# Kernel tuning notes

Measured on AMD Instinct MI355X. Metric: run time of the kernel, lower is better.

The kernel has to match this reference:

```python
import jax, jax.numpy as jnp
import numpy as np
from jax import lax

# ---- module hyperparams (match init_kwargs and mamba_ssm Mamba2 defaults) ----
D_MODEL = 768
D_STATE = 64
D_CONV = 4
EXPAND = 2
HEADDIM = 64  # Mamba2 default
D_INNER = EXPAND * D_MODEL          # 1536
NHEADS = D_INNER // HEADDIM         # 24
NGROUPS = 1
CONV_DIM = D_INNER + 2 * NGROUPS * D_STATE          # 1664
D_IN_PROJ = 2 * D_INNER + 2 * NGROUPS * D_STATE + NHEADS  # 3224
BSZ, SEQ = 2, 512
EPS = 1e-5


def setup_inputs() -> dict:
    key = jax.random.key(0)
    ks = jax.random.split(key, 12)
    def n(k, shape, s):
        return jax.random.normal(k, shape, jnp.float32) * s
    x = n(ks[0], (BSZ, SEQ, D_MODEL), 1.0)
    in_proj_w = n(ks[1], (D_IN_PROJ, D_MODEL), D_MODEL ** -0.5)
    conv_w = n(ks[2], (CONV_DIM, D_CONV), D_CONV ** -0.5)
    conv_b = jnp.zeros((CONV_DIM,), jnp.float32)
    # dt_bias = softplus^{-1}(dt) with dt log-uniform in [1e-3, 1e-1] (Mamba2 init)
    dt = jnp.exp(jax.random.uniform(ks[3], (NHEADS,), jnp.float32,
                                    minval=np.log(1e-3), maxval=np.log(1e-1)))
    dt_bias = dt + jnp.log(-jnp.expm1(-dt))
    A_log = jnp.log(jax.random.uniform(ks[4], (NHEADS,), jnp.float32, minval=1.0, maxval=16.0))
    D_param = jnp.ones((NHEADS,), jnp.float32)
    norm_w = jnp.ones((D_INNER,), jnp.float32)
    out_proj_w = n(ks[5], (D_MODEL, D_INNER), D_INNER ** -0.5)
    ln1_w = jnp.ones((D_MODEL,), jnp.float32); ln1_b = jnp.zeros((D_MODEL,), jnp.float32)
    ln2_w = jnp.ones((D_MODEL,), jnp.float32); ln2_b = jnp.zeros((D_MODEL,), jnp.float32)
    ff_w1 = n(ks[6], (4 * D_MODEL, D_MODEL), D_MODEL ** -0.5)
    ff_b1 = jnp.zeros((4 * D_MODEL,), jnp.float32)
    ff_w2 = n(ks[7], (D_MODEL, 4 * D_MODEL), (4 * D_MODEL) ** -0.5)
    ff_b2 = jnp.zeros((D_MODEL,), jnp.float32)
    return dict(x=x, in_proj_w=in_proj_w, conv_w=conv_w, conv_b=conv_b,
                dt_bias=dt_bias, A_log=A_log, D_param=D_param, norm_w=norm_w,
                out_proj_w=out_proj_w, ln1_w=ln1_w, ln1_b=ln1_b,
                ln2_w=ln2_w, ln2_b=ln2_b, ff_w1=ff_w1, ff_b1=ff_b1,
                ff_w2=ff_w2, ff_b2=ff_b2)


def layernorm(x, w, b):
    mu = jnp.mean(x, -1, keepdims=True)
    xc = x - mu
    var = jnp.mean(xc * xc, -1, keepdims=True)
    return xc * lax.rsqrt(var + EPS) * w + b


def mamba2(xn, in_proj_w, conv_w, conv_b, dt_bias, A_log, D_param, norm_w, out_proj_w):
    b, l, _ = xn.shape
    zxbcdt = xn @ in_proj_w.T  # [b, l, D_IN_PROJ]
    z = zxbcdt[..., :D_INNER]
    xBC = zxbcdt[..., D_INNER:D_INNER + CONV_DIM]
    dt = zxbcdt[..., D_INNER + CONV_DIM:]
    # causal depthwise conv over time on xBC
    xc = lax.conv_general_dilated(xBC.transpose(0, 2, 1), conv_w[:, None, :], (1,),
                                  [(D_CONV - 1, 0)], dimension_numbers=('NCH', 'OIH', 'NCH'),
                                  feature_group_count=CONV_DIM)
    xBC = jax.nn.silu((xc + conv_b[None, :, None]).transpose(0, 2, 1))
    xs = xBC[..., :D_INNER].reshape(b, l, NHEADS, HEADDIM)
    Bm = xBC[..., D_INNER:D_INNER + D_STATE]   # [b, l, n]  (ngroups=1)
    Cm = xBC[..., D_INNER + D_STATE:]          # [b, l, n]
    dt = jax.nn.softplus(dt + dt_bias)         # [b, l, h]
    dA = jnp.exp(dt * (-jnp.exp(A_log)))       # [b, l, h]
    dBx = jnp.einsum('blh,bln,blhp->blhpn', dt, Bm, xs)
    def step(h, inp):
        dA_t, dBx_t = inp                      # [b,h], [b,h,p,n]
        h = dA_t[:, :, None, None] * h + dBx_t
        return h, h
    _, hs = lax.scan(step, jnp.zeros((b, NHEADS, HEADDIM, D_STATE), xn.dtype),
                     (dA.transpose(1, 0, 2), dBx.transpose(1, 0, 2, 3, 4)))
    y = jnp.einsum('lbhpn,bln->blhp', hs, Cm) + D_param[None, None, :, None] * xs
    y = y.reshape(b, l, D_INNER) * jax.nn.silu(z)   # gated RMSNorm (norm_before_gate=False)
    y = y * lax.rsqrt(jnp.mean(y * y, -1, keepdims=True) + EPS) * norm_w
    return y @ out_proj_w.T


def reference(x, in_proj_w, conv_w, conv_b, dt_bias, A_log, D_param, norm_w,
              out_proj_w, ln1_w, ln1_b, ln2_w, ln2_b, ff_w1, ff_b1, ff_w2, ff_b2):
    residual = x
    xn = layernorm(x, ln1_w, ln1_b)
    mp = (in_proj_w, conv_w, conv_b, dt_bias, A_log, D_param, norm_w, out_proj_w)
    out_f = mamba2(xn, *mp)
    out_b = jnp.flip(mamba2(jnp.flip(xn, 1), *mp), 1)
    m = layernorm(out_f + out_b, ln2_w, ln2_b)
    ff = jax.nn.gelu(m @ ff_w1.T + ff_b1, approximate=False) @ ff_w2.T + ff_b2
    return ff + residual
```

## Files before the change

kernel.cpp:

```cpp
#include <hip/hip_runtime.h>
#include <hip/hip_bf16.h>
#include <math.h>

#define SEQ     512
#define BSZ     2
#define ROWS    (BSZ*SEQ)
#define DMODEL  768
#define DINNER  1536
#define DSTATE  64
#define NHEADS  24
#define HEADDIM 64
#define CONVDIM 1664
#define DINPROJ 3224
#define DFF     3072
#define EPSF    1e-5f

typedef __attribute__((ext_vector_type(8))) short s16x8;
typedef __attribute__((ext_vector_type(4))) float f32x4;

__device__ __forceinline__ float b2f(const __hip_bfloat16 v){ return __bfloat162float(v); }
__device__ __forceinline__ __hip_bfloat16 f2b(float v){ return __float2bfloat16(v); }
__device__ __forceinline__ ushort f2bu(float v){
  union { __hip_bfloat16 b; ushort u; } c; c.b = __float2bfloat16(v); return c.u;
}
__device__ __forceinline__ float u2f(ushort u){ return __uint_as_float(((uint)u) << 16); }

__device__ __forceinline__ void gload16(const void* g, void* l){
  __builtin_amdgcn_global_load_lds((__attribute__((address_space(1))) const void*)g,
                                   (__attribute__((address_space(3))) void*)l, 16, 0, 0);
}

__device__ __forceinline__ float block_sum256(float v, float* sh){
  #pragma unroll
  for (int off = 32; off > 0; off >>= 1) v += __shfl_down(v, off, 64);
  int w = threadIdx.x >> 6;
  if ((threadIdx.x & 63) == 0) sh[w] = v;
  __syncthreads();
  float t = sh[0] + sh[1] + sh[2] + sh[3];
  __syncthreads();
  return t;
}

__global__ __launch_bounds__(256) void zerof_kernel(float* out, int n){
  int i = blockIdx.x*256 + threadIdx.x;
  if (i < n) out[i] = 0.f;
}

__global__ __launch_bounds__(256) void prep_kernel(const float* __restrict__ w0,
    const float* __restrict__ w1, const float* __restrict__ w2,
    const float* __restrict__ w3, ushort* __restrict__ o,
    int n0, int n1, int n2, int n3, int wblocks,
    const float* __restrict__ xin, const float* __restrict__ lnw,
    const float* __restrict__ lnb, __hip_bfloat16* __restrict__ xnout)
{
  __shared__ float sh[4];
  if ((int)blockIdx.x < wblocks){
    int i = (blockIdx.x*256 + threadIdx.x) << 2;
    int total = n0 + n1 + n2 + n3;
    if (i < total){
      const float* s; int off;
      if      (i < n0)       { s = w0; off = i; }
      else if (i < n0+n1)    { s = w1; off = i - n0; }
      else if (i < n0+n1+n2) { s = w2; off = i - n0 - n1; }
      else                   { s = w3; off = i - n0 - n1 - n2; }
      float4 f = *(const float4*)(s + off);
      *(ushort4*)(o + i) = make_ushort4(f2bu(f.x), f2bu(f.y), f2bu(f.z), f2bu(f.w));
    }
    return;
  }
  const int row = blockIdx.x - wblocks;
  const float* xr = xin + (size_t)row * DMODEL;
  float v[3]; float s = 0.f;
  #pragma unroll
  for (int i = 0; i < 3; i++){ int c = threadIdx.x + i*256; v[i] = xr[c]; s += v[i]; }
  s = block_sum256(s, sh);
  float mu = s * (1.f/DMODEL);
  float s2 = 0.f;
  #pragma unroll
  for (int i = 0; i < 3; i++){ float d = v[i]-mu; s2 += d*d; }
  s2 = block_sum256(s2, sh);
  float rs = rsqrtf(s2*(1.f/DMODEL) + EPSF);
  #pragma unroll
  for (int i = 0; i < 3; i++){
    int c = threadIdx.x + i*256;
    xnout[(size_t)row*DMODEL + c] = f2b((v[i]-mu)*rs*lnw[c] + lnb[c]);
  }
}

__global__ __launch_bounds__(256) void ln_kernel(const float* __restrict__ in,
    const float* __restrict__ w, const float* __restrict__ b,
    __hip_bfloat16* __restrict__ out)
{
  __shared__ float sh[4];
  const int row = blockIdx.x;
  const float* xr = in + (size_t)row * DMODEL;
  float v[3]; float s = 0.f;
  #pragma unroll
  for (int i = 0; i < 3; i++){ int c = threadIdx.x + i*256; v[i] = xr[c]; s += v[i]; }
  s = block_sum256(s, sh);
  float mu = s * (1.f/DMODEL);
  float s2 = 0.f;
  #pragma unroll
  for (int i = 0; i < 3; i++){ float d = v[i]-mu; s2 += d*d; }
  s2 = block_sum256(s2, sh);
  float rs = rsqrtf(s2*(1.f/DMODEL) + EPSF);
  #pragma unroll
  for (int i = 0; i < 3; i++){
    int c = threadIdx.x + i*256;
    out[(size_t)row*DMODEL + c] = f2b((v[i]-mu)*rs*w[c] + b[c]);
  }
}

__device__ __forceinline__ s16x8 ld_frag(const ushort* p){
  union { ushort4 h[2]; s16x8 v; } u;
  u.h[0] = *(const ushort4*)(p);
  u.h[1] = *(const ushort4*)(p + 4);
  return u.v;
}

template<typename CTy, int KS, int EPI>
__global__ __launch_bounds__(256) void gemm_bb64(const __hip_bfloat16* __restrict__ A_,
    const __hip_bfloat16* __restrict__ B_, CTy* __restrict__ C,
    const float* __restrict__ bias, int M, int N, int K)
{
  __shared__ __align__(16) ushort As[3][64][64];
  __shared__ __align__(16) ushort Bs[3][64][64];
  const int tid  = threadIdx.x;
  const int lane = tid & 63, wave = tid >> 6;
  const int wr = wave >> 1, wc = wave & 1;
  const int n0 = blockIdx.x * 64, m0 = blockIdx.y * 64;
  const int Kc   = K / KS;
  const int kbeg = blockIdx.z * Kc;
  const int NT   = Kc >> 6;
  const int srw  = lane >> 3;
  const int scol = (((lane & 7) ^ srw) << 3);
  const int l15  = lane & 15;
  const int r7   = l15 & 7;
  const int c0   = lane >> 4;

  const ushort* Au = (const ushort*)A_;
  const ushort* Bu = (const ushort*)B_;

  f32x4 acc[2][2] = {};

  auto stage = [&](int bf, int k0){
    #pragma unroll
    for (int q = 0; q < 2; q++){
      int row = q*32 + wave*8 + srw;
      gload16(Au + (size_t)(m0 + row)*K + kbeg + k0 + scol, &As[bf][q*32 + wave*8][0]);
      int nr = n0 + row; if (nr > N-1) nr = N-1;
      gload16(Bu + (size_t)nr*K + kbeg + k0 + scol, &Bs[bf][q*32 + wave*8][0]);
    }
  };

  stage(0, 0);
  stage(1, 64);
  asm volatile("s_waitcnt vmcnt(4)" ::: "memory");
  __builtin_amdgcn_s_barrier();

  for (int t = 0; t < NT; ++t){
    const int nxt = t + 2;
    if (nxt < NT) stage(nxt % 3, nxt << 6);
    const int cur = t % 3;
    #pragma unroll
    for (int tt = 0; tt < 2; tt++){
      const int fc = (((tt*4 + c0) ^ r7) << 3);
      s16x8 a0 = ld_frag(&As[cur][wr*32      + l15][fc]);
      s16x8 a1 = ld_frag(&As[cur][wr*32 + 16 + l15][fc]);
      s16x8 b0 = ld_frag(&Bs[cur][wc*32      + l15][fc]);
      s16x8 b1 = ld_frag(&Bs[cur][wc*32 + 16 + l15][fc]);
      acc[0][0] = __builtin_amdgcn_mfma_f32_16x16x32_bf16(a0, b0, acc[0][0], 0, 0, 0);
      acc[0][1] = __builtin_amdgcn_mfma_f32_16x16x32_bf16(a0, b1, acc[0][1], 0, 0, 0);
      acc[1][0] = __builtin_amdgcn_mfma_f32_16x16x32_bf16(a1, b0, acc[1][0], 0, 0, 0);
      acc[1][1] = __builtin_amdgcn_mfma_f32_16x16x32_bf16(a1, b1, acc[1][1], 0, 0, 0);
    }
    if (t == NT-1) break;
    if (nxt < NT) { asm volatile("s_waitcnt vmcnt(4)" ::: "memory"); }
    else          { asm volatile("s_waitcnt vmcnt(0)" ::: "memory"); }
    __builtin_amdgcn_s_barrier();
  }

  CTy* Cz = C + (size_t)blockIdx.z * M * N;
  const int crow = (lane >> 4) * 4;
  #pragma unroll
  for (int i = 0; i < 2; i++){
    #pragma unroll
    for (int j = 0; j < 2; j++){
      int col = n0 + wc*32 + j*16 + l15;
      if (col < N){
        #pragma unroll
        for (int q = 0; q < 4; q++){
          int rowg = m0 + wr*32 + i*16 + crow + q;
          if constexpr (EPI == 1){
            float v = acc[i][j][q] + bias[col];
            Cz[(size_t)rowg*N + col] = (CTy)f2b(0.5f * v * (1.f + erff(v * 0.70710678118654752f)));
          } else if constexpr (sizeof(CTy) == 4){
            Cz[(size_t)rowg*N + col] = acc[i][j][q];
          } else {
            Cz[(size_t)rowg*N + col] = (CTy)f2b(acc[i][j][q]);
          }
        }
      }
    }
  }
}

template<typename CTy>
__global__ __launch_bounds__(256) void gemm_mfma(const __hip_bfloat16* __restrict__ A,
    const float* __restrict__ B, CTy* __restrict__ C, int M, int N, int K)
{
  __shared__ __align__(16) ushort As[64][72];
  __shared__ __align__(16) ushort Bs[64][72];
  const int tid  = threadIdx.x;
  const int lane = tid & 63, wave = tid >> 6;
  const int wr = wave >> 1, wc = wave & 1;
  const int n0 = blockIdx.x * 64, m0 = blockIdx.y * 64;
  const int sr = tid >> 2;
  const int sc = (tid & 3) * 16;
  const int l15 = lane & 15, lk = (lane >> 4) * 8;

  f32x4 acc[2][2] = {};

  const ushort* Au = (const ushort*)A;
  int nr = n0 + sr; if (nr > N-1) nr = N-1;

  for (int k0 = 0; k0 < K; k0 += 64){
    const ushort* ag = Au + (size_t)(m0 + sr)*K + (k0 + sc);
    ushort4 a0 = *(const ushort4*)(ag);
    ushort4 a1 = *(const ushort4*)(ag + 4);
    ushort4 a2 = *(const ushort4*)(ag + 8);
    ushort4 a3 = *(const ushort4*)(ag + 12);
    const float* bg = B + (size_t)nr*K + (k0 + sc);
    float4 f0 = *(const float4*)(bg);
    float4 f1 = *(const float4*)(bg + 4);
    float4 f2 = *(const float4*)(bg + 8);
    float4 f3 = *(const float4*)(bg + 12);
    ushort4 b0 = make_ushort4(f2bu(f0.x), f2bu(f0.y), f2bu(f0.z), f2bu(f0.w));
    ushort4 b1 = make_ushort4(f2bu(f1.x), f2bu(f1.y), f2bu(f1.z), f2bu(f1.w));
    ushort4 b2 = make_ushort4(f2bu(f2.x), f2bu(f2.y), f2bu(f2.z), f2bu(f2.w));
    ushort4 b3 = make_ushort4(f2bu(f3.x), f2bu(f3.y), f2bu(f3.z), f2bu(f3.w));

    __syncthreads();
    *(ushort4*)&As[sr][sc +  0] = a0;
    *(ushort4*)&As[sr][sc +  4] = a1;
    *(ushort4*)&As[sr][sc +  8] = a2;
    *(ushort4*)&As[sr][sc + 12] = a3;
    *(ushort4*)&Bs[sr][sc +  0] = b0;
    *(ushort4*)&Bs[sr][sc +  4] = b1;
    *(ushort4*)&Bs[sr][sc +  8] = b2;
    *(ushort4*)&Bs[sr][sc + 12] = b3;
    __syncthreads();

    #pragma unroll
    for (int kk = 0; kk < 64; kk += 32){
      s16x8 af0 = ld_frag(&As[wr*32      + l15][kk + lk]);
      s16x8 af1 = ld_frag(&As[wr*32 + 16 + l15][kk + lk]);
      s16x8 bf0 = ld_frag(&Bs[wc*32      + l15][kk + lk]);
      s16x8 bf1 = ld_frag(&Bs[wc*32 + 16 + l15][kk + lk]);
      acc[0][0] = __builtin_amdgcn_mfma_f32_16x16x32_bf16(af0, bf0, acc[0][0], 0, 0, 0);
      acc[0][1] = __builtin_amdgcn_mfma_f32_16x16x32_bf16(af0, bf1, acc[0][1], 0, 0, 0);
      acc[1][0] = __builtin_amdgcn_mfma_f32_16x16x32_bf16(af1, bf0, acc[1][0], 0, 0, 0);
      acc[1][1] = __builtin_amdgcn_mfma_f32_16x16x32_bf16(af1, bf1, acc[1][1], 0, 0, 0);
    }
  }

  const int crow = (lane >> 4) * 4;
  #pragma unroll
  for (int i = 0; i < 2; i++){
    #pragma unroll
    for (int j = 0; j < 2; j++){
      int col = n0 + wc*32 + j*16 + l15;
      if (col < N){
        #pragma unroll
        for (int q = 0; q < 4; q++){
          int rowg = m0 + wr*32 + i*16 + crow + q;
          if constexpr (sizeof(CTy) == 4) C[(size_t)rowg*N + col] = acc[i][j][q];
          else                            C[(size_t)rowg*N + col] = (CTy)f2b(acc[i][j][q]);
        }
      }
    }
  }
}

__global__ __launch_bounds__(256) void convdt_kernel(const __hip_bfloat16* __restrict__ zx,
    const float* __restrict__ cw, const float* __restrict__ cb,
    const float* __restrict__ dt_bias, const float* __restrict__ A_log,
    __hip_bfloat16* __restrict__ xconv, float* __restrict__ dtb, float* __restrict__ dab)
{
  const int tt = blockIdx.x, b = blockIdx.y, dir = blockIdx.z;
  const int c8 = threadIdx.x * 8;
  if (c8 < CONVDIM){
    size_t rowoff[4]; bool ok[4];
    #pragma unroll
    for (int k = 0; k < 4; k++){
      int s = tt - 3 + k;
      ok[k] = (s >= 0);
      int ss = ok[k] ? s : 0;
      int phys = dir ? (SEQ-1-ss) : ss;
      rowoff[k] = ((size_t)(b*SEQ + phys))*DINPROJ + DINNER + c8;
    }
    float acc[8];
    {
      float4 cb0 = *(const float4*)(cb + c8);
      float4 cb1 = *(const float4*)(cb + c8 + 4);
      acc[0]=cb0.x; acc[1]=cb0.y; acc[2]=cb0.z; acc[3]=cb0.w;
      acc[4]=cb1.x; acc[5]=cb1.y; acc[6]=cb1.z; acc[7]=cb1.w;
    }
    float wv[8][4];
    #pragma unroll
    for (int j = 0; j < 8; j++){
      float4 w4 = *(const float4*)(cw + (size_t)(c8 + j)*4);
      wv[j][0]=w4.x; wv[j][1]=w4.y; wv[j][2]=w4.z; wv[j][3]=w4.w;
    }
    const ushort* zu = (const ushort*)zx;
    #pragma unroll
    for (int k = 0; k < 4; k++){
      if (ok[k]){
        ushort4 v0 = *(const ushort4*)(zu + rowoff[k]);
        ushort4 v1 = *(const ushort4*)(zu + rowoff[k] + 4);
        acc[0] = fmaf(wv[0][k], u2f(v0.x), acc[0]);
        acc[1] = fmaf(wv[1][k], u2f(v0.y), acc[1]);
        acc[2] = fmaf(wv[2][k], u2f(v0.z), acc[2]);
        acc[3] = fmaf(wv[3][k], u2f(v0.w), acc[3]);
        acc[4] = fmaf(wv[4][k], u2f(v1.x), acc[4]);
        acc[5] = fmaf(wv[5][k], u2f(v1.y), acc[5]);
        acc[6] = fmaf(wv[6][k], u2f(v1.z), acc[6]);
        acc[7] = fmaf(wv[7][k], u2f(v1.w), acc[7]);
      }
    }
    ushort* outr = (ushort*)xconv + ((size_t)((dir*BSZ + b)*SEQ + tt))*CONVDIM + c8;
    ushort o[8];
    #pragma unroll
    for (int j = 0; j < 8; j++){
      float s = acc[j] / (1.f + expf(-acc[j]));
      o[j] = f2bu(s);
    }
    *(ushort4*)(outr)     = make_ushort4(o[0],o[1],o[2],o[3]);
    *(ushort4*)(outr + 4) = make_ushort4(o[4],o[5],o[6],o[7]);
  }
  if (dir == 0 && threadIdx.x < NHEADS){
    int h = threadIdx.x;
    size_t r = (size_t)b*SEQ + tt;
    float raw = b2f(zx[r*DINPROJ + (DINNER + CONVDIM) + h]) + dt_bias[h];
    float sp  = fmaxf(raw, 0.f) + log1pf(expf(-fabsf(raw)));
    dtb[r*NHEADS + h] = sp;
    dab[r*NHEADS + h] = expf(-sp * expf(A_log[h]));
  }
}

#define CT 16

__global__ __launch_bounds__(256) void scan_pass1(const __hip_bfloat16* __restrict__ xconv,
    const float* __restrict__ dtb, const float* __restrict__ dab,
    float* __restrict__ stateBuf, int CL)
{
  const int c = blockIdx.x, h = blockIdx.y, z = blockIdx.z;
  const int b = z & 1, dir = z >> 1;
  const int tid = threadIdx.x, lane = tid & 63, wave = tid >> 6, nb = wave * 16;
  __shared__ __align__(16) float Bc[CT][64], Xc[CT][64];
  __shared__ float dAc[CT], dtc[CT];
  float hreg[16];
  #pragma unroll
  for (int j = 0; j < 16; j++) hreg[j] = 0.f;
  const size_t dirbase = (size_t)z * SEQ;
  const int cstart = c * CL;

  const int ttl = tid >> 4, c4 = (tid & 15) << 2;

  for (int c0 = cstart; c0 < cstart + CL; c0 += CT){
    {
      const ushort* rowp = (const ushort*)xconv + (dirbase + c0 + ttl)*(size_t)CONVDIM;
      ushort4 bv = *(const ushort4*)(rowp + DINNER + c4);
      ushort4 xv = *(const ushort4*)(rowp + h*HEADDIM + c4);
      Bc[ttl][c4+0] = u2f(bv.x); Bc[ttl][c4+1] = u2f(bv.y);
      Bc[ttl][c4+2] = u2f(bv.z); Bc[ttl][c4+3] = u2f(bv.w);
      Xc[ttl][c4+0] = u2f(xv.x); Xc[ttl][c4+1] = u2f(xv.y);
      Xc[ttl][c4+2] = u2f(xv.z); Xc[ttl][c4+3] = u2f(xv.w);
    }
    if (tid < CT){
      int phys = dir ? (SEQ-1 - (c0 + tid)) : (c0 + tid);
      size_t r = (size_t)b*SEQ + phys;
      dAc[tid] = dab[r*NHEADS + h];
      dtc[tid] = dtb[r*NHEADS + h];
    }
    __syncthreads();

    #pragma unroll 4
    for (int tt = 0; tt < CT; tt++){
      float dA = dAc[tt];
      float dtx = dtc[tt] * Xc[tt][lane];
      const float4* Bq = (const float4*)&Bc[tt][nb];
      float4 B0 = Bq[0], B1 = Bq[1], B2 = Bq[2], B3 = Bq[3];
      hreg[ 0]=fmaf(dA,hreg[ 0],dtx*B0.x); hreg[ 1]=fmaf(dA,hreg[ 1],dtx*B0.y);
      hreg[ 2]=fmaf(dA,hreg[ 2],dtx*B0.z); hreg[ 3]=fmaf(dA,hreg[ 3],dtx*B0.w);
      hreg[ 4]=fmaf(dA,hreg[ 4],dtx*B1.x); hreg[ 5]=fmaf(dA,hreg[ 5],dtx*B1.y);
      hreg[ 6]=fmaf(dA,hreg[ 6],dtx*B1.z); hreg[ 7]=fmaf(dA,hreg[ 7],dtx*B1.w);
      hreg[ 8]=fmaf(dA,hreg[ 8],dtx*B2.x); hreg[ 9]=fmaf(dA,hreg[ 9],dtx*B2.y);
      hreg[10]=fmaf(dA,hreg[10],dtx*B2.z); hreg[11]=fmaf(dA,hreg[11],dtx*B2.w);
      hreg[12]=fmaf(dA,hreg[12],dtx*B3.x); hreg[13]=fmaf(dA,hreg[13],dtx*B3.y);
      hreg[14]=fmaf(dA,hreg[14],dtx*B3.z); hreg[15]=fmaf(dA,hreg[15],dtx*B3.w);
    }
    __syncthreads();
  }

  float* sp = stateBuf + (((size_t)c*4 + z)*NHEADS + h)*4096 + (size_t)lane*64 + nb;
  *(float4*)(sp +  0) = make_float4(hreg[ 0],hreg[ 1],hreg[ 2],hreg[ 3]);
  *(float4*)(sp +  4) = make_float4(hreg[ 4],hreg[ 5],hreg[ 6],hreg[ 7]);
  *(float4*)(sp +  8) = make_float4(hreg[ 8],hreg[ 9],hreg[10],hreg[11]);
  *(float4*)(sp + 12) = make_float4(hreg[12],hreg[13],hreg[14],hreg[15]);
}

__global__ __launch_bounds__(256) void scan_pass2(const __hip_bfloat16* __restrict__ xconv,
    const __hip_bfloat16* __restrict__ zx, const float* __restrict__ dtb,
    const float* __restrict__ dab, const float* __restrict__ Dp,
    const float* __restrict__ stateBuf, __hip_bfloat16* __restrict__ yg, int CL)
{
  const int c = blockIdx.x, h = blockIdx.y, z = blockIdx.z;
  const int b = z & 1, dir = z >> 1;
  const int tid = threadIdx.x, lane = tid & 63, wave = tid >> 6, nb = wave * 16;
  __shared__ __align__(16) float Bc[CT][64], Cc[CT][64], Xc[CT][64];
  __shared__ __align__(16) float Yp[4][CT][64];
  __shared__ float dAc[CT], dtc[CT];
  __shared__ float sP[8];
  float hreg[16];
  #pragma unroll
  for (int j = 0; j < 16; j++) hreg[j] = 0.f;
  if (c > 0){
    if (tid < c){
      float p = 1.f;
      for (int i = 0; i < CL; i++){
        int t = tid*CL + i;
        int phys = dir ? (SEQ-1 - t) : t;
        p *= dab[((size_t)b*SEQ + phys)*NHEADS + h];
      }
      sP[tid] = p;
    }
    __syncthreads();
    float suffix = 1.f;
    for (int i = c-1; i >= 0; --i){
      const float* sp = stateBuf + (((size_t)i*4 + z)*NHEADS + h)*4096 + (size_t)lane*64 + nb;
      float4 s0 = *(const float4*)(sp+0), s1 = *(const float4*)(sp+4);
      float4 s2 = *(const float4*)(sp+8), s3 = *(const float4*)(sp+12);
      hreg[ 0]=fmaf(suffix,s0.x,hreg[ 0]); hreg[ 1]=fmaf(suffix,s0.y,hreg[ 1]);
      hreg[ 2]=fmaf(suffix,s0.z,hreg[ 2]); hreg[ 3]=fmaf(suffix,s0.w,hreg[ 3]);
      hreg[ 4]=fmaf(suffix,s1.x,hreg[ 4]); hreg[ 5]=fmaf(suffix,s1.y,hreg[ 5]);
      hreg[ 6]=fmaf(suffix,s1.z,hreg[ 6]); hreg[ 7]=fmaf(suffix,s1.w,hreg[ 7]);
      hreg[ 8]=fmaf(suffix,s2.x,hreg[ 8]); hreg[ 9]=fmaf(suffix,s2.y,hreg[ 9]);
      hreg[10]=fmaf(suffix,s2.z,hreg[10]); hreg[11]=fmaf(suffix,s2.w,hreg[11]);
      hreg[12]=fmaf(suffix,s3.x,hreg[12]); hreg[13]=fmaf(suffix,s3.y,hreg[13]);
      hreg[14]=fmaf(suffix,s3.z,hreg[14]); hreg[15]=fmaf(suffix,s3.w,hreg[15]);
      suffix *= sP[i];
    }
    __syncthreads();
  }
  const float Dh = Dp[h];
  const size_t dirbase = (size_t)z * SEQ;
  const int cstart = c * CL;
  const int ttl = tid >> 4, c4 = (tid & 15) << 2;

  for (int c0 = cstart; c0 < cstart + CL; c0 += CT){
    {
      const ushort* rowp = (const ushort*)xconv + (dirbase + c0 + ttl)*(size_t)CONVDIM;
      ushort4 bv = *(const ushort4*)(rowp + DINNER + c4);
      ushort4 cv = *(const ushort4*)(rowp + DINNER + DSTATE + c4);
      ushort4 xv = *(const ushort4*)(rowp + h*HEADDIM + c4);
      Bc[ttl][c4+0] = u2f(bv.x); Bc[ttl][c4+1] = u2f(bv.y);
      Bc[ttl][c4+2] = u2f(bv.z); Bc[ttl][c4+3] = u2f(bv.w);
      Cc[ttl][c4+0] = u2f(cv.x); Cc[ttl][c4+1] = u2f(cv.y);
      Cc[ttl][c4+2] = u2f(cv.z); Cc[ttl][c4+3] = u2f(cv.w);
      Xc[ttl][c4+0] = u2f(xv.x); Xc[ttl][c4+1] = u2f(xv.y);
      Xc[ttl][c4+2] = u2f(xv.z); Xc[ttl][c4+3] = u2f(xv.w);
    }
    if (tid < CT){
      int phys = dir ? (SEQ-1 - (c0 + tid)) : (c0 + tid);
      size_t r = (size_t)b*SEQ + phys;
      dAc[tid] = dab[r*NHEADS + h];
      dtc[tid] = dtb[r*NHEADS + h];
    }
    __syncthreads();

    #pragma unroll 4
    for (int tt = 0; tt < CT; tt++){
      float dA = dAc[tt];
      float dtx = dtc[tt] * Xc[tt][lane];
      const float4* Bq = (const float4*)&Bc[tt][nb];
      const float4* Cq = (const float4*)&Cc[tt][nb];
      float4 B0 = Bq[0], B1 = Bq[1], B2 = Bq[2], B3 = Bq[3];
      float4 C0 = Cq[0], C1 = Cq[1], C2 = Cq[2], C3 = Cq[3];
      float y0 = 0.f, y1 = 0.f, y2 = 0.f, y3 = 0.f;
      hreg[ 0]=fmaf(dA,hreg[ 0],dtx*B0.x); y0=fmaf(hreg[ 0],C0.x,y0);
      hreg[ 1]=fmaf(dA,hreg[ 1],dtx*B0.y); y1=fmaf(hreg[ 1],C0.y,y1);
      hreg[ 2]=fmaf(dA,hreg[ 2],dtx*B0.z); y2=fmaf(hreg[ 2],C0.z,y2);
      hreg[ 3]=fmaf(dA,hreg[ 3],dtx*B0.w); y3=fmaf(hreg[ 3],C0.w,y3);
      hreg[ 4]=fmaf(dA,hreg[ 4],dtx*B1.x); y0=fmaf(hreg[ 4],C1.x,y0);
      hreg[ 5]=fmaf(dA,hreg[ 5],dtx*B1.y); y1=fmaf(hreg[ 5],C1.y,y1);
      hreg[ 6]=fmaf(dA,hreg[ 6],dtx*B1.z); y2=fmaf(hreg[ 6],C1.z,y2);
      hreg[ 7]=fmaf(dA,hreg[ 7],dtx*B1.w); y3=fmaf(hreg[ 7],C1.w,y3);
      hreg[ 8]=fmaf(dA,hreg[ 8],dtx*B2.x); y0=fmaf(hreg[ 8],C2.x,y0);
      hreg[ 9]=fmaf(dA,hreg[ 9],dtx*B2.y); y1=fmaf(hreg[ 9],C2.y,y1);
      hreg[10]=fmaf(dA,hreg[10],dtx*B2.z); y2=fmaf(hreg[10],C2.z,y2);
      hreg[11]=fmaf(dA,hreg[11],dtx*B2.w); y3=fmaf(hreg[11],C2.w,y3);
      hreg[12]=fmaf(dA,hreg[12],dtx*B3.x); y0=fmaf(hreg[12],C3.x,y0);
      hreg[13]=fmaf(dA,hreg[13],dtx*B3.y); y1=fmaf(hreg[13],C3.y,y1);
      hreg[14]=fmaf(dA,hreg[14],dtx*B3.z); y2=fmaf(hreg[14],C3.z,y2);
      hreg[15]=fmaf(dA,hreg[15],dtx*B3.w); y3=fmaf(hreg[15],C3.w,y3);
      Yp[wave][tt][lane] = (y0+y1) + (y2+y3);
    }
    __syncthreads();

    {
      int tl = tid >> 4, p4 = (tid & 15) << 2;
      float4 ya = *(const float4*)&Yp[0][tl][p4];
      float4 yb4 = *(const float4*)&Yp[1][tl][p4];
      float4 yc = *(const float4*)&Yp[2][tl][p4];
      float4 yd = *(const float4*)&Yp[3][tl][p4];
      float4 xv = *(const float4*)&Xc[tl][p4];
      int phys = dir ? (SEQ-1 - (c0 + tl)) : (c0 + tl);
      size_t r = (size_t)b*SEQ + phys;
      const ushort* zp = (const ushort*)zx + r*DINPROJ + h*HEADDIM + p4;
      ushort4 zv = *(const ushort4*)zp;
      float zf[4] = { u2f(zv.x), u2f(zv.y), u2f(zv.z), u2f(zv.w) };
      float yv[4] = { ya.x+yb4.x+yc.x+yd.x + Dh*xv.x,
                      ya.y+yb4.y+yc.y+yd.y + Dh*xv.y,
                      ya.z+yb4.z+yc.z+yd.z + Dh*xv.z,
                      ya.w+yb4.w+yc.w+yd.w + Dh*xv.w };
      ushort o[4];
      #pragma unroll
      for (int j = 0; j < 4; j++){
        float sil = zf[j] / (1.f + expf(-zf[j]));
        o[j] = f2bu(yv[j] * sil);
      }
      ushort* op = (ushort*)yg + ((size_t)dir*ROWS + r)*DINNER + h*HEADDIM + p4;
      *(ushort4*)op = make_ushort4(o[0],o[1],o[2],o[3]);
    }
    __syncthreads();
  }
}

__global__ __launch_bounds__(256) void rmscomb_kernel(const __hip_bfloat16* __restrict__ yg,
    const float* __restrict__ nw, __hip_bfloat16* __restrict__ u)
{
  __shared__ float sh[4];
  const int row = blockIdx.x;
  const __hip_bfloat16* yf = yg + (size_t)row*DINNER;
  const __hip_bfloat16* yb = yg + (size_t)(ROWS + row)*DINNER;
  float vf[6], vb[6]; float sf = 0.f, sb = 0.f;
  #pragma unroll
  for (int i = 0; i < 6; i++){
    int c = threadIdx.x + i*256;
    vf[i] = b2f(yf[c]); sf += vf[i]*vf[i];
    vb[i] = b2f(yb[c]); sb += vb[i]*vb[i];
  }
  sf = block_sum256(sf, sh);
  sb = block_sum256(sb, sh);
  float rf = rsqrtf(sf*(1.f/DINNER) + EPSF);
  float rb = rsqrtf(sb*(1.f/DINNER) + EPSF);
  #pragma unroll
  for (int i = 0; i < 6; i++){
    int c = threadIdx.x + i*256;
    u[(size_t)row*DINNER + c] = f2b((vf[i]*rf + vb[i]*rb) * nw[c]);
  }
}

template<int NP>
__global__ __launch_bounds__(256) void ln2_kernel(const float* __restrict__ in,
    size_t pstride, const float* __restrict__ w, const float* __restrict__ b,
    __hip_bfloat16* __restrict__ out)
{
  __shared__ float sh[4];
  const int row = blockIdx.x;
  float v[3]; float s = 0.f;
  #pragma unroll
  for (int i = 0; i < 3; i++){
    int c = threadIdx.x + i*256;
    size_t idx = (size_t)row*DMODEL + c;
    float t = 0.f;
    #pragma unroll
    for (int p = 0; p < NP; p++) t += in[p*pstride + idx];
    v[i] = t; s += t;
  }
  s = block_sum256(s, sh);
  float mu = s * (1.f/DMODEL);
  float s2 = 0.f;
  #pragma unroll
  for (int i = 0; i < 3; i++){ float d = v[i]-mu; s2 += d*d; }
  s2 = block_sum256(s2, sh);
  float rs = rsqrtf(s2*(1.f/DMODEL) + EPSF);
  #pragma unroll
  for (int i = 0; i < 3; i++){
    int c = threadIdx.x + i*256;
    out[(size_t)row*DMODEL + c] = f2b((v[i]-mu)*rs*w[c] + b[c]);
  }
}

__global__ __launch_bounds__(256) void gelu_kernel(const __hip_bfloat16* __restrict__ g,
    const float* __restrict__ b1, __hip_bfloat16* __restrict__ out)
{
  size_t idx = (size_t)blockIdx.x*256 + threadIdx.x;
  int c = (int)(idx % DFF);
  float v = b2f(g[idx]) + b1[c];
  out[idx] = f2b(0.5f * v * (1.f + erff(v * 0.70710678118654752f)));
}

template<int NP>
__global__ __launch_bounds__(256) void final_kernel(const float* __restrict__ f,
    size_t pstride, const float* __restrict__ bias, const float* __restrict__ x,
    float* __restrict__ out)
{
  size_t i4 = ((size_t)blockIdx.x*256 + threadIdx.x) << 2;
  int c = (int)(i4 % DMODEL);
  float4 bv = *(const float4*)(bias + c);
  float4 xv = *(const float4*)(x + i4);
  float4 s = make_float4(bv.x+xv.x, bv.y+xv.y, bv.z+xv.z, bv.w+xv.w);
  #pragma unroll
  for (int p = 0; p < NP; p++){
    float4 fv = *(const float4*)(f + p*pstride + i4);
    s.x += fv.x; s.y += fv.y; s.z += fv.z; s.w += fv.w;
  }
  *(float4*)(out + i4) = s;
}

extern "C" void kernel_launch(void* const* d_in, const int* in_sizes, int n_in,
                              void* d_out, int out_size, void* d_ws, size_t ws_size,
                              hipStream_t stream)
{
  float* out = (float*)d_out;

  const size_t NEED = 19906560;
  if (ws_size < NEED || n_in < 17){
    zerof_kernel<<<(out_size + 255)/256, 256, 0, stream>>>(out, out_size);
    return;
  }

  const float* x       = (const float*)d_in[0];
  const float* in_proj_w = (const float*)d_in[1];
  const float* conv_w  = (const float*)d_in[2];
  const float* conv_b  = (const float*)d_in[3];
  const float* dt_bias = (const float*)d_in[4];
  const float* A_log   = (const float*)d_in[5];
  const float* D_param = (const float*)d_in[6];
  const float* norm_w  = (const float*)d_in[7];
  const float* out_proj_w = (const float*)d_in[8];
  const float* ln1_w   = (const float*)d_in[9];
  const float* ln1_b   = (const float*)d_in[10];
  const float* ln2_w   = (const float*)d_in[11];
  const float* ln2_b   = (const float*)d_in[12];
  const float* ff_w1   = (const float*)d_in[13];
  const float* ff_b1   = (const float*)d_in[14];
  const float* ff_w2   = (const float*)d_in[15];
  const float* ff_b2   = (const float*)d_in[16];

  char* ws = (char*)d_ws;
  __hip_bfloat16* zx  = (__hip_bfloat16*)(ws + 0);
  __hip_bfloat16* xn  = (__hip_bfloat16*)(ws + 6602752);
  float*          dtb = (float*)(ws + 6602752);
  float*          dab = (float*)(ws + 6701056);
  __hip_bfloat16* xcv = (__hip_bfloat16*)(ws + 6799360);
  __hip_bfloat16* yg  = (__hip_bfloat16*)(ws + 13615104);
  __hip_bfloat16* u   = (__hip_bfloat16*)(ws + 0);
  float*          mo  = (float*)(ws + 3145728);
  __hip_bfloat16* mb  = (__hip_bfloat16*)(ws + 0);
  __hip_bfloat16* g   = (__hip_bfloat16*)(ws + 6799360);
  __hip_bfloat16* gb  = (__hip_bfloat16*)(ws + 13615104);
  float*          fo  = (float*)(ws + 0);

  const size_t WBALL = 16748544;
  const size_t PARTS = 12582912;
  const size_t CHB   = 1572864;
  const size_t PSTRIDE = (size_t)ROWS * DMODEL;
  const int WN_IN  = DINPROJ*DMODEL;
  const int WN_OUT = DMODEL*DINNER;
  const int WN_F1  = DFF*DMODEL;
  const int WN_F2  = DMODEL*DFF;

  size_t rem = ws_size - NEED;
  bool fast = (rem >= WBALL + PARTS);
  ushort* wb    = (ushort*)(ws + NEED);
  float*  parts = (float*) (ws + NEED + WBALL);
  size_t scanoff = NEED + (fast ? (WBALL + PARTS) : 0);
  size_t srem = ws_size - scanoff;
  int NC = 1;
  if      (srem >= 8*CHB) NC = 8;
  else if (srem >= 4*CHB) NC = 4;
  else if (srem >= 2*CHB) NC = 2;
  float* stateBuf = (float*)(ws + scanoff);
  const int CL = SEQ / NC;

  if (fast){
    const int wblocks = (WN_IN + WN_OUT + WN_F1 + WN_F2) / 4 / 256;
    prep_kernel<<<wblocks + ROWS, 256, 0, stream>>>(in_proj_w, out_proj_w, ff_w1, ff_w2,
        wb, WN_IN, WN_OUT, WN_F1, WN_F2, wblocks, x, ln1_w, ln1_b, xn);
    gemm_bb64<__hip_bfloat16,1,0><<<dim3((DINPROJ+63)/64, ROWS/64), 256, 0, stream>>>(
        xn, (const __hip_bfloat16*)wb, zx, nullptr, ROWS, DINPROJ, DMODEL);
  } else {
    ln_kernel<<<ROWS, 256, 0, stream>>>(x, ln1_w, ln1_b, xn);
    gemm_mfma<<<dim3((DINPROJ+63)/64, ROWS/64), 256, 0, stream>>>(xn, in_proj_w, zx, ROWS, DINPROJ, DMODEL);
  }
  convdt_kernel<<<dim3(SEQ, BSZ, 2), 256, 0, stream>>>(zx, conv_w, conv_b, dt_bias, A_log, xcv, dtb, dab);
  if (NC > 1){
    scan_pass1<<<dim3(NC-1, NHEADS, 4), 256, 0, stream>>>(xcv, dtb, dab, stateBuf, CL);
  }
  scan_pass2<<<dim3(NC, NHEADS, 4), 256, 0, stream>>>(xcv, zx, dtb, dab, D_param, stateBuf, yg, CL);
  rmscomb_kernel<<<ROWS, 256, 0, stream>>>(yg, norm_w, u);
  if (fast){
    gemm_bb64<float,2,0><<<dim3(DMODEL/64, ROWS/64, 2), 256, 0, stream>>>(
        u, (const __hip_bfloat16*)(wb + WN_IN), parts, nullptr, ROWS, DMODEL, DINNER);
    ln2_kernel<2><<<ROWS, 256, 0, stream>>>(parts, PSTRIDE, ln2_w, ln2_b, mb);
  } else {
    gemm_mfma<<<dim3(DMODEL/64, ROWS/64), 256, 0, stream>>>(u, out_proj_w, mo, ROWS, DMODEL, DINNER);
    ln2_kernel<1><<<ROWS, 256, 0, stream>>>(mo, 0, ln2_w, ln2_b, mb);
  }
  if (fast){
    gemm_bb64<__hip_bfloat16,1,1><<<dim3(DFF/64, ROWS/64), 256, 0, stream>>>(
        mb, (const __hip_bfloat16*)(wb + WN_IN + WN_OUT), gb, ff_b1, ROWS, DFF, DMODEL);
  } else {
    gemm_mfma<<<dim3(DFF/64, ROWS/64), 256, 0, stream>>>(mb, ff_w1, g, ROWS, DFF, DMODEL);
    gelu_kernel<<<(ROWS*DFF)/256, 256, 0, stream>>>(g, ff_b1, gb);
  }
  if (fast){
    gemm_bb64<float,4,0><<<dim3(DMODEL/64, ROWS/64, 4), 256, 0, stream>>>(
        gb, (const __hip_bfloat16*)(wb + WN_IN + WN_OUT + WN_F1), parts, nullptr, ROWS, DMODEL, DFF);
    final_kernel<4><<<(ROWS*DMODEL/4)/256, 256, 0, stream>>>(parts, PSTRIDE, ff_b2, x, out);
  } else {
    gemm_mfma<<<dim3(DMODEL/64, ROWS/64), 256, 0, stream>>>(gb, ff_w2, fo, ROWS, DMODEL, DFF);
    final_kernel<1><<<(ROWS*DMODEL/4)/256, 256, 0, stream>>>(fo, 0, ff_b2, x, out);
  }
}
```

Baseline: 268.9 us.

## Add scan fixup kernel for sequential chunk-state propagation and allow 16 chunks

```diff
diff --git a/kernel.cpp b/kernel.cpp
--- a/kernel.cpp
+++ b/kernel.cpp
@@ -410,6 +410,51 @@
   *(float4*)(sp + 12) = make_float4(hreg[12],hreg[13],hreg[14],hreg[15]);
 }
 
+__global__ __launch_bounds__(256) void scan_fixup(const float* __restrict__ dab,
+    float* __restrict__ stateBuf, int NC, int CL)
+{
+  const int h = blockIdx.x, z = blockIdx.y;
+  const int b = z & 1, dir = z >> 1;
+  const int tid = threadIdx.x;
+  __shared__ float sdA[SEQ];
+  __shared__ float P[16];
+  for (int i = tid; i < SEQ; i += 256){
+    int phys = dir ? (SEQ-1-i) : i;
+    sdA[i] = dab[((size_t)b*SEQ + phys)*NHEADS + h];
+  }
+  __syncthreads();
+  if (tid < NC){
+    float p = 1.f;
+    for (int i = 0; i < CL; i++) p *= sdA[tid*CL + i];
+    P[tid] = p;
+  }
+  __syncthreads();
+
+  float hrun[16], Lcur[16];
+  #pragma unroll
+  for (int j = 0; j < 16; j++) hrun[j] = 0.f;
+  {
+    const float* s0 = stateBuf + ((size_t)z*NHEADS + h)*4096 + (size_t)tid*16;
+    #pragma unroll
+    for (int j = 0; j < 16; j++) Lcur[j] = s0[j];
+  }
+  for (int c = 1; c < NC; c++){
+    float Pp = P[c-1];
+    float hnew[16];
+    #pragma unroll
+    for (int j = 0; j < 16; j++) hnew[j] = fmaf(Pp, hrun[j], Lcur[j]);
+    float* sc = stateBuf + (((size_t)c*4 + z)*NHEADS + h)*4096 + (size_t)tid*16;
+    if (c < NC-1){
+      #pragma unroll
+      for (int j = 0; j < 16; j++) Lcur[j] = sc[j];
+    }
+    #pragma unroll
+    for (int j = 0; j < 16; j++) sc[j] = hnew[j];
+    #pragma unroll
+    for (int j = 0; j < 16; j++) hrun[j] = hnew[j];
+  }
+}
+
 __global__ __launch_bounds__(256) void scan_pass2(const __hip_bfloat16* __restrict__ xconv,
     const __hip_bfloat16* __restrict__ zx, const float* __restrict__ dtb,
     const float* __restrict__ dab, const float* __restrict__ Dp,
@@ -421,37 +466,18 @@
   __shared__ __align__(16) float Bc[CT][64], Cc[CT][64], Xc[CT][64];
   __shared__ __align__(16) float Yp[4][CT][64];
   __shared__ float dAc[CT], dtc[CT];
-  __shared__ float sP[8];
   float hreg[16];
-  #pragma unroll
-  for (int j = 0; j < 16; j++) hreg[j] = 0.f;
-  if (c > 0){
-    if (tid < c){
-      float p = 1.f;
-      for (int i = 0; i < CL; i++){
-        int t = tid*CL + i;
-        int phys = dir ? (SEQ-1 - t) : t;
-        p *= dab[((size_t)b*SEQ + phys)*NHEADS + h];
-      }
-      sP[tid] = p;
-    }
-    __syncthreads();
-    float suffix = 1.f;
-    for (int i = c-1; i >= 0; --i){
-      const float* sp = stateBuf + (((size_t)i*4 + z)*NHEADS + h)*4096 + (size_t)lane*64 + nb;
-      float4 s0 = *(const float4*)(sp+0), s1 = *(const float4*)(sp+4);
-      float4 s2 = *(const float4*)(sp+8), s3 = *(const float4*)(sp+12);
-      hreg[ 0]=fmaf(suffix,s0.x,hreg[ 0]); hreg[ 1]=fmaf(suffix,s0.y,hreg[ 1]);
-      hreg[ 2]=fmaf(suffix,s0.z,hreg[ 2]); hreg[ 3]=fmaf(suffix,s0.w,hreg[ 3]);
-      hreg[ 4]=fmaf(suffix,s1.x,hreg[ 4]); hreg[ 5]=fmaf(suffix,s1.y,hreg[ 5]);
-      hreg[ 6]=fmaf(suffix,s1.z,hreg[ 6]); hreg[ 7]=fmaf(suffix,s1.w,hreg[ 7]);
-      hreg[ 8]=fmaf(suffix,s2.x,hreg[ 8]); hreg[ 9]=fmaf(suffix,s2.y,hreg[ 9]);
-      hreg[10]=fmaf(suffix,s2.z,hreg[10]); hreg[11]=fmaf(suffix,s2.w,hreg[11]);
-      hreg[12]=fmaf(suffix,s3.x,hreg[12]); hreg[13]=fmaf(suffix,s3.y,hreg[13]);
-      hreg[14]=fmaf(suffix,s3.z,hreg[14]); hreg[15]=fmaf(suffix,s3.w,hreg[15]);
-      suffix *= sP[i];
-    }
-    __syncthreads();
+  if (c == 0){
+    #pragma unroll
+    for (int j = 0; j < 16; j++) hreg[j] = 0.f;
+  } else {
+    const float* sp = stateBuf + (((size_t)c*4 + z)*NHEADS + h)*4096 + (size_t)lane*64 + nb;
+    float4 s0 = *(const float4*)(sp+0), s1 = *(const float4*)(sp+4);
+    float4 s2 = *(const float4*)(sp+8), s3 = *(const float4*)(sp+12);
+    hreg[ 0]=s0.x; hreg[ 1]=s0.y; hreg[ 2]=s0.z; hreg[ 3]=s0.w;
+    hreg[ 4]=s1.x; hreg[ 5]=s1.y; hreg[ 6]=s1.z; hreg[ 7]=s1.w;
+    hreg[ 8]=s2.x; hreg[ 9]=s2.y; hreg[10]=s2.z; hreg[11]=s2.w;
+    hreg[12]=s3.x; hreg[13]=s3.y; hreg[14]=s3.z; hreg[15]=s3.w;
   }
   const float Dh = Dp[h];
   const size_t dirbase = (size_t)z * SEQ;
@@ -680,9 +706,10 @@
   size_t scanoff = NEED + (fast ? (WBALL + PARTS) : 0);
   size_t srem = ws_size - scanoff;
   int NC = 1;
-  if      (srem >= 8*CHB) NC = 8;
-  else if (srem >= 4*CHB) NC = 4;
-  else if (srem >= 2*CHB) NC = 2;
+  if      (srem >= 16*CHB) NC = 16;
+  else if (srem >=  8*CHB) NC = 8;
+  else if (srem >=  4*CHB) NC = 4;
+  else if (srem >=  2*CHB) NC = 2;
   float* stateBuf = (float*)(ws + scanoff);
   const int CL = SEQ / NC;
 
@@ -699,6 +726,7 @@
   convdt_kernel<<<dim3(SEQ, BSZ, 2), 256, 0, stream>>>(zx, conv_w, conv_b, dt_bias, A_log, xcv, dtb, dab);
   if (NC > 1){
     scan_pass1<<<dim3(NC-1, NHEADS, 4), 256, 0, stream>>>(xcv, dtb, dab, stateBuf, CL);
+    scan_fixup<<<dim3(NHEADS, 4), 256, 0, stream>>>(dab, stateBuf, NC, CL);
   }
   scan_pass2<<<dim3(NC, NHEADS, 4), 256, 0, stream>>>(xcv, zx, dtb, dab, D_param, stateBuf, yg, CL);
   rmscomb_kernel<<<ROWS, 256, 0, stream>>>(yg, norm_w, u);
```

Measured after the change: 267.7 us. About the same (-0.5%).
